# Optimization experiments

Measured on AMD Instinct MI355X. Metric: run time of the kernel, lower is better.

The kernel has to match this reference:

```python
import jax, jax.numpy as jnp
import numpy as np

N = 100000   # nodes
E = 3200000  # edges (before self-loops)
IN, H, OUT = 128, 256, 40

def glorot(key, shape):
    lim = (6.0 / (shape[0] + shape[1])) ** 0.5
    return jax.random.uniform(key, shape, jnp.float32, -lim, lim)

def setup_inputs() -> dict:
    key = jax.random.key(0)
    ks = jax.random.split(key, 8)
    x = jax.random.normal(ks[0], (N, IN), jnp.float32)
    edge_index = jax.random.randint(ks[1], (2, E), 0, N, dtype=jnp.int32)
    return {
        "x": x,
        "edge_index": edge_index,
        "W0": glorot(ks[2], (IN, H)),  "b0": jnp.zeros((H,), jnp.float32),
        "W1": glorot(ks[3], (H, H)),   "b1": jnp.zeros((H,), jnp.float32),
        "W2": glorot(ks[4], (H, OUT)), "b2": jnp.zeros((OUT,), jnp.float32),
    }

def _gcn_norm(edge_index, n):
    # PyG gcn_norm: add self-loops, symmetric D^{-1/2} A D^{-1/2}
    loops = jnp.arange(n, dtype=edge_index.dtype)
    src = jnp.concatenate([edge_index[0], loops])
    dst = jnp.concatenate([edge_index[1], loops])
    deg = jax.ops.segment_sum(jnp.ones_like(src, jnp.float32), dst, num_segments=n)
    dinv = jnp.where(deg > 0, jax.lax.rsqrt(deg), 0.0)
    norm = dinv[src] * dinv[dst]  # [E+N]
    return src, dst, norm

def _gcn_layer(h, W, b, src, dst, norm, n):
    h = h @ W                                   # transform first (PyG order)
    msg = h[src] * norm[:, None]                # gather + scale
    agg = jax.ops.segment_sum(msg, dst, num_segments=n)  # scatter-add
    return agg + b

def reference(x, edge_index, W0, b0, W1, b1, W2, b2):
    n = x.shape[0]
    src, dst, norm = _gcn_norm(edge_index, n)
    h = jnp.tanh(_gcn_layer(x, W0, b0, src, dst, norm, n))  # dropout = identity (eval)
    h = jnp.tanh(_gcn_layer(h, W1, b1, src, dst, norm, n))
    out = _gcn_layer(h, W2, b2, src, dst, norm, n)
    return jax.nn.log_softmax(out, axis=1)
```

## Files before the change

kernel.cpp:

```cpp
#include <hip/hip_runtime.h>
#include <hip/hip_bf16.h>
#include <cmath>


typedef unsigned short u16;
typedef __attribute__((ext_vector_type(8))) short short8;
typedef __attribute__((ext_vector_type(4))) float f32x4;

#define BSHIFT 10
#define BNODES (1 << BSHIFT)
#define ECAP   36864
#define BMASK 0x00FF00FFu

__device__ __forceinline__ u16 f2bf(float f) {
    unsigned int u = __float_as_uint(f);
    u += 0x7fffu + ((u >> 16) & 1u);
    return (u16)(u >> 16);
}
__device__ __forceinline__ float bflo(unsigned int u) { return __uint_as_float(u << 16); }
__device__ __forceinline__ float bfhi(unsigned int u) { return __uint_as_float(u & 0xffff0000u); }

__device__ __forceinline__ int q8(float v) {
    return (int)rintf(fminf(fmaxf(v, -127.0f), 127.0f));
}


__global__ __launch_bounds__(128) void init_gcur_kernel(
        int* __restrict__ gcur, int nb) {
    int b = blockIdx.x * 128 + threadIdx.x;
    if (b < nb) gcur[b] = b * ECAP;
}

__global__ __launch_bounds__(256) void bucketize_kernel(
        const int* __restrict__ src, const int* __restrict__ dst,
        int* __restrict__ gcur, unsigned int* __restrict__ ebuf, int E) {
    __shared__ int cnt[128];
    __shared__ int base[128];
    int tid = threadIdx.x;
    int chunk0 = blockIdx.x * 8192;
    int cend = min(chunk0 + 8192, E);
    for (int r0 = chunk0; r0 < cend; r0 += 2048) {
        if (tid < 128) cnt[tid] = 0;
        __syncthreads();
        int rank[8], bk[8];
        unsigned int pk[8];
#pragma unroll
        for (int j = 0; j < 8; j++) {
            int e = r0 + j * 256 + tid;
            bk[j] = -1;
            if (e < cend) {
                int d = dst[e];
                bk[j] = d >> BSHIFT;
                pk[j] = (unsigned int)src[e] | ((unsigned int)(d & (BNODES - 1)) << 17);
                rank[j] = atomicAdd(&cnt[bk[j]], 1);
            }
        }
        __syncthreads();
        if (tid < 128 && cnt[tid] > 0) base[tid] = atomicAdd(&gcur[tid], cnt[tid]);
        __syncthreads();
#pragma unroll
        for (int j = 0; j < 8; j++)
            if (bk[j] >= 0) ebuf[base[bk[j]] + rank[j]] = pk[j];
        __syncthreads();
    }
}

__global__ __launch_bounds__(256) void deg_hist_kernel(
        const unsigned int* __restrict__ ebuf, const int* __restrict__ gcur,
        int* __restrict__ degi, int N) {
    __shared__ int h[BNODES];
    int b = blockIdx.x;
    int nb0 = b << BSHIFT;
    int nodes = min(BNODES, N - nb0);
    for (int i = threadIdx.x; i < nodes; i += 256) h[i] = 0;
    __syncthreads();
    int estart = b * ECAP;
    int eend = gcur[b];
    for (int e = estart + threadIdx.x; e < eend; e += 256)
        atomicAdd(&h[ebuf[e] >> 17], 1);
    __syncthreads();
    for (int i = threadIdx.x; i < nodes; i += 256) degi[nb0 + i] = h[i];
}

__global__ __launch_bounds__(256) void dinv_kernel(
        const int* __restrict__ degi, float* __restrict__ dinv, int n) {
    int i = blockIdx.x * 256 + threadIdx.x;
    if (i < n) dinv[i] = rsqrtf((float)degi[i] + 1.0f);
}

__global__ __launch_bounds__(256) void scan_part_kernel(
        const int* __restrict__ deg, int* __restrict__ part, int n) {
    __shared__ int s[256];
    int i = blockIdx.x * 256 + threadIdx.x;
    s[threadIdx.x] = (i < n) ? deg[i] : 0;
    __syncthreads();
    for (int off = 128; off; off >>= 1) {
        if (threadIdx.x < off) s[threadIdx.x] += s[threadIdx.x + off];
        __syncthreads();
    }
    if (threadIdx.x == 0) part[blockIdx.x] = s[0];
}

__global__ __launch_bounds__(1024) void scan_top_kernel(
        int* __restrict__ part, int nb) {
    __shared__ int s[1024];
    int t = threadIdx.x;
    int v = (t < nb) ? part[t] : 0;
    s[t] = v;
    __syncthreads();
    for (int off = 1; off < 1024; off <<= 1) {
        int u = (t >= off) ? s[t - off] : 0;
        __syncthreads();
        s[t] += u;
        __syncthreads();
    }
    if (t < nb) part[t] = s[t] - v;
}

__global__ __launch_bounds__(256) void scan_apply_kernel(
        const int* __restrict__ deg, const int* __restrict__ part,
        int* __restrict__ rs, int n) {
    __shared__ int s[256];
    int i = blockIdx.x * 256 + threadIdx.x;
    int v = (i < n) ? deg[i] : 0;
    s[threadIdx.x] = v;
    __syncthreads();
    for (int off = 1; off < 256; off <<= 1) {
        int u = (threadIdx.x >= off) ? s[threadIdx.x - off] : 0;
        __syncthreads();
        s[threadIdx.x] += u;
        __syncthreads();
    }
    if (i < n) rs[i] = part[blockIdx.x] + s[threadIdx.x] - v;
}

__global__ __launch_bounds__(256) void csr_fill_kernel(
        const unsigned int* __restrict__ ebuf, const int* __restrict__ gcur,
        const int* __restrict__ rs, int* __restrict__ csr, int N) {
    __shared__ int lcur[BNODES];
    int b = blockIdx.x;
    int nb0 = b << BSHIFT;
    int nodes = min(BNODES, N - nb0);
    for (int i = threadIdx.x; i < nodes; i += 256) lcur[i] = rs[nb0 + i];
    __syncthreads();
    int estart = b * ECAP;
    int eend = gcur[b];
    for (int e = estart + threadIdx.x; e < eend; e += 256) {
        unsigned int v = ebuf[e];
        int s = v & 0x1FFFF;
        int dl = v >> 17;
        int pos = atomicAdd(&lcur[dl], 1);
        csr[pos] = s;
    }
}

__global__ __launch_bounds__(256) void wt_kernel(
        const float* __restrict__ W, u16* __restrict__ Wt, int K, int NC) {
    int i = blockIdx.x * 256 + threadIdx.x;
    if (i < K * NC) {
        int k = i / NC, c = i % NC;
        Wt[(size_t)c * K + k] = f2bf(W[i]);
    }
}

__global__ __launch_bounds__(256) void scale_x_kernel(
        const float* __restrict__ x, const float* __restrict__ dinv,
        unsigned int* __restrict__ out, int total4) {
    int i = blockIdx.x * 256 + threadIdx.x;
    if (i >= total4) return;
    int n = i >> 5;
    float4 v = reinterpret_cast<const float4*>(x)[i];
    float s = dinv[n] * 63.5f;
    int a0 = q8(v.x * s), a1 = q8(v.y * s), a2 = q8(v.z * s), a3 = q8(v.w * s);
    out[i] = (unsigned int)(a0 & 0xff) | ((unsigned int)(a1 & 0xff) << 8) |
             ((unsigned int)(a2 & 0xff) << 16) | ((unsigned int)(a3 & 0xff) << 24);
}

#define ACC8(q0, q1)                                                  \
    do {                                                              \
        aex += (q0) & BMASK; aox += ((q0) >> 8) & BMASK;              \
        aey += (q1) & BMASK; aoy += ((q1) >> 8) & BMASK;              \
    } while (0)

__global__ __launch_bounds__(256) void agg128_i8_kernel(
        const signed char* __restrict__ in, u16* __restrict__ out,
        const int* __restrict__ rs, const int* __restrict__ deg,
        const int* __restrict__ csr, const float* __restrict__ dinv, int n) {
    int wid = blockIdx.x * 4 + (threadIdx.x >> 6);
    if (wid >= n) return;
    int lane = threadIdx.x & 63;
    int quad = lane >> 4;
    int l16 = lane & 15;
    int start = rs[wid];
    int cnt = deg[wid];

    unsigned int aex = 0, aox = 0, aey = 0, aoy = 0;
    if (quad == 0) {
        uint2 q = *reinterpret_cast<const uint2*>(
            in + (size_t)wid * 128 + l16 * 8);
        q.x ^= 0x80808080u; q.y ^= 0x80808080u;
        ACC8(q.x, q.y);
    }
    int i = 0;
    for (; i + 16 <= cnt; i += 16) {
        int s[4];
#pragma unroll
        for (int j = 0; j < 4; j++) s[j] = csr[start + i + 4 * j + quad];
#pragma unroll
        for (int j = 0; j < 4; j++) {
            uint2 q = *reinterpret_cast<const uint2*>(
                in + (size_t)s[j] * 128 + l16 * 8);
            q.x ^= 0x80808080u; q.y ^= 0x80808080u;
            ACC8(q.x, q.y);
        }
    }
    for (; i + 4 <= cnt; i += 4) {
        int s0 = csr[start + i + quad];
        uint2 q = *reinterpret_cast<const uint2*>(
            in + (size_t)s0 * 128 + l16 * 8);
        q.x ^= 0x80808080u; q.y ^= 0x80808080u;
        ACC8(q.x, q.y);
    }
    int rem = cnt - i;
    if (quad < rem) {
        int s0 = csr[start + i + quad];
        uint2 q = *reinterpret_cast<const uint2*>(
            in + (size_t)s0 * 128 + l16 * 8);
        q.x ^= 0x80808080u; q.y ^= 0x80808080u;
        ACC8(q.x, q.y);
    }
    aex += (unsigned int)__shfl((int)aex, lane + 32);
    aox += (unsigned int)__shfl((int)aox, lane + 32);
    aey += (unsigned int)__shfl((int)aey, lane + 32);
    aoy += (unsigned int)__shfl((int)aoy, lane + 32);
    aex += (unsigned int)__shfl((int)aex, lane + 16);
    aox += (unsigned int)__shfl((int)aox, lane + 16);
    aey += (unsigned int)__shfl((int)aey, lane + 16);
    aoy += (unsigned int)__shfl((int)aoy, lane + 16);
    if (lane < 16) {
        int T = cnt + 1;
        int bias = 128 * T;
        float c = dinv[wid] * (2.0f / 127.0f);
        float f0 = (float)((int)(aex & 0xFFFFu) - bias) * c;
        float f1 = (float)((int)(aox & 0xFFFFu) - bias) * c;
        float f2 = (float)((int)(aex >> 16) - bias) * c;
        float f3 = (float)((int)(aox >> 16) - bias) * c;
        float f4 = (float)((int)(aey & 0xFFFFu) - bias) * c;
        float f5 = (float)((int)(aoy & 0xFFFFu) - bias) * c;
        float f6 = (float)((int)(aey >> 16) - bias) * c;
        float f7 = (float)((int)(aoy >> 16) - bias) * c;
        uint4 o;
        o.x = (unsigned)f2bf(f0) | ((unsigned)f2bf(f1) << 16);
        o.y = (unsigned)f2bf(f2) | ((unsigned)f2bf(f3) << 16);
        o.z = (unsigned)f2bf(f4) | ((unsigned)f2bf(f5) << 16);
        o.w = (unsigned)f2bf(f6) | ((unsigned)f2bf(f7) << 16);
        reinterpret_cast<uint4*>(out + (size_t)wid * 128)[l16] = o;
    }
}

__global__ __launch_bounds__(256) void agg_i8_kernel(
        const signed char* __restrict__ in, u16* __restrict__ out,
        const int* __restrict__ rs, const int* __restrict__ deg,
        const int* __restrict__ csr, const float* __restrict__ dinv, int n) {
    int wid = blockIdx.x * 4 + (threadIdx.x >> 6);
    if (wid >= n) return;
    int lane = threadIdx.x & 63;
    int start = rs[wid];
    int cnt = deg[wid];

    unsigned int q = *reinterpret_cast<const unsigned int*>(
        in + (size_t)wid * 256 + lane * 4) ^ 0x80808080u;
    unsigned int ae = q & BMASK, ao = (q >> 8) & BMASK;

    int i = 0;
    for (; i + 16 <= cnt; i += 16) {
        int s[16];
#pragma unroll
        for (int j = 0; j < 16; j++)
            s[j] = __builtin_amdgcn_readfirstlane(csr[start + i + j]);
        unsigned int qq[16];
#pragma unroll
        for (int j = 0; j < 16; j++)
            qq[j] = *reinterpret_cast<const unsigned int*>(
                in + (size_t)s[j] * 256 + lane * 4);
#pragma unroll
        for (int j = 0; j < 16; j++) {
            unsigned int v = qq[j] ^ 0x80808080u;
            ae += v & BMASK;
            ao += (v >> 8) & BMASK;
        }
    }
    if (i < cnt) {
        int s[16];
#pragma unroll
        for (int j = 0; j < 16; j++) {
            int e = i + j;
            e = (e < cnt) ? e : (cnt - 1);
            s[j] = __builtin_amdgcn_readfirstlane(csr[start + e]);
        }
        unsigned int qq[16];
#pragma unroll
        for (int j = 0; j < 16; j++)
            qq[j] = *reinterpret_cast<const unsigned int*>(
                in + (size_t)s[j] * 256 + lane * 4);
#pragma unroll
        for (int j = 0; j < 16; j++) {
            unsigned int m = (i + j < cnt) ? 0xFFFFFFFFu : 0u;
            unsigned int v = (qq[j] ^ 0x80808080u) & m;
            ae += v & BMASK;
            ao += (v >> 8) & BMASK;
        }
    }

    int bias = 128 * (cnt + 1);
    float c = dinv[wid] * (1.0f / 127.0f);
    float f0 = (float)((int)(ae & 0xFFFFu) - bias) * c;
    float f1 = (float)((int)(ao & 0xFFFFu) - bias) * c;
    float f2 = (float)((int)(ae >> 16) - bias) * c;
    float f3 = (float)((int)(ao >> 16) - bias) * c;
    uint2 o;
    o.x = (unsigned)f2bf(f0) | ((unsigned)f2bf(f1) << 16);
    o.y = (unsigned)f2bf(f2) | ((unsigned)f2bf(f3) << 16);
    reinterpret_cast<uint2*>(out + (size_t)wid * 256)[lane] = o;
}

template<int EPI, typename CT>
__global__ __launch_bounds__(256) void mfma_mm_kernel(
        const u16* __restrict__ A, const u16* __restrict__ Bt,
        CT* __restrict__ C, int M, int K, int NC,
        const float* __restrict__ bias, const float* __restrict__ postscale,
        float qs) {
    __shared__ u16 As[128 * 40];
    __shared__ u16 Bs[64 * 40];
    int t = threadIdx.x;
    int w = t >> 6, lane = t & 63, quad = lane >> 4, l16 = lane & 15;
    int row0 = blockIdx.x * 128;
    int col0 = blockIdx.y * 64;

    f32x4 acc[2][4];
#pragma unroll
    for (int s = 0; s < 2; s++)
#pragma unroll
        for (int nb = 0; nb < 4; nb++)
            acc[s][nb] = (f32x4){0.f, 0.f, 0.f, 0.f};

    int bn = t >> 2, bkq = (t & 3) << 3;
    for (int k0 = 0; k0 < K; k0 += 32) {
#pragma unroll
        for (int i = t; i < 512; i += 256) {
            int r = i >> 2, c = (i & 3) << 3;
            int gr = row0 + r;
            uint4 v = {0u, 0u, 0u, 0u};
            if (gr < M)
                v = *reinterpret_cast<const uint4*>(A + (size_t)gr * K + k0 + c);
            *reinterpret_cast<uint4*>(&As[r * 40 + c]) = v;
        }
        {
            int gc = col0 + bn;
            uint4 v = {0u, 0u, 0u, 0u};
            if (gc < NC)
                v = *reinterpret_cast<const uint4*>(Bt + (size_t)gc * K + k0 + bkq);
            *reinterpret_cast<uint4*>(&Bs[bn * 40 + bkq]) = v;
        }
        __syncthreads();

        short8 af[2], bf[4];
        af[0] = *reinterpret_cast<const short8*>(&As[(w * 32 + l16) * 40 + quad * 8]);
        af[1] = *reinterpret_cast<const short8*>(&As[(w * 32 + 16 + l16) * 40 + quad * 8]);
#pragma unroll
        for (int nb = 0; nb < 4; nb++)
            bf[nb] = *reinterpret_cast<const short8*>(&Bs[(nb * 16 + l16) * 40 + quad * 8]);
#pragma unroll
        for (int s = 0; s < 2; s++)
#pragma unroll
            for (int nb = 0; nb < 4; nb++)
                acc[s][nb] = __builtin_amdgcn_mfma_f32_16x16x32_bf16(
                    af[s], bf[nb], acc[s][nb], 0, 0, 0);
        __syncthreads();
    }

#pragma unroll
    for (int s = 0; s < 2; s++) {
        int rbase = row0 + w * 32 + s * 16 + quad * 4;
#pragma unroll
        for (int nb = 0; nb < 4; nb++) {
            int gc = col0 + nb * 16 + l16;
#pragma unroll
            for (int r = 0; r < 4; r++) {
                int gr = rbase + r;
                if (gr >= M || gc >= NC) continue;
                float v = acc[s][nb][r];
                if constexpr (EPI == 1) v = tanhf(v + bias[gc]);
                else                    v = v * postscale[gr];
                if constexpr (sizeof(CT) == 1) {
                    float m = qs;
                    if constexpr (EPI == 1) m *= postscale[gr];
                    C[(size_t)gr * NC + gc] = (CT)q8(v * m);
                } else {
                    C[(size_t)gr * NC + gc] = (CT)f2bf(v);
                }
            }
        }
    }
}

__global__ __launch_bounds__(256) void agg40_ls_kernel(
        const signed char* __restrict__ in, const int* __restrict__ rs,
        const int* __restrict__ deg, const int* __restrict__ csr,
        const float* __restrict__ dinv, const float* __restrict__ bias,
        float* __restrict__ out, int n) {
    int wid = blockIdx.x * 4 + (threadIdx.x >> 6);
    if (wid >= n) return;
    int lane = threadIdx.x & 63;
    int grp = lane / 5;
    int l5 = lane - grp * 5;
    bool act = lane < 60;
    int start = rs[wid];
    int cnt = deg[wid];

    unsigned int aex = 0, aox = 0, aey = 0, aoy = 0;
    if (lane < 5) {
        uint2 q = *reinterpret_cast<const uint2*>(
            in + (size_t)wid * 40 + l5 * 8);
        q.x ^= 0x80808080u; q.y ^= 0x80808080u;
        ACC8(q.x, q.y);
    }
    for (int base = 0; base < cnt; base += 12) {
        int e = base + grp;
        if (act && e < cnt) {
            int s0 = csr[start + e];
            uint2 q = *reinterpret_cast<const uint2*>(
                in + (size_t)s0 * 40 + l5 * 8);
            q.x ^= 0x80808080u; q.y ^= 0x80808080u;
            ACC8(q.x, q.y);
        }
    }
    aex += (unsigned int)__shfl((int)aex, lane + 30);
    aox += (unsigned int)__shfl((int)aox, lane + 30);
    aey += (unsigned int)__shfl((int)aey, lane + 30);
    aoy += (unsigned int)__shfl((int)aoy, lane + 30);
    aex += (unsigned int)__shfl((int)aex, lane + 15);
    aox += (unsigned int)__shfl((int)aox, lane + 15);
    aey += (unsigned int)__shfl((int)aey, lane + 15);
    aoy += (unsigned int)__shfl((int)aoy, lane + 15);
    aex += (unsigned int)__shfl((int)aex, lane + 5) + (unsigned int)__shfl((int)aex, lane + 10);
    aox += (unsigned int)__shfl((int)aox, lane + 5) + (unsigned int)__shfl((int)aox, lane + 10);
    aey += (unsigned int)__shfl((int)aey, lane + 5) + (unsigned int)__shfl((int)aey, lane + 10);
    aoy += (unsigned int)__shfl((int)aoy, lane + 5) + (unsigned int)__shfl((int)aoy, lane + 10);

    bool act5 = lane < 5;
    float s = dinv[wid];
    float v0 = -INFINITY, v1 = -INFINITY, v2 = -INFINITY, v3 = -INFINITY;
    float v4 = -INFINITY, v5 = -INFINITY, v6 = -INFINITY, v7 = -INFINITY;
    if (act5) {
        int bb = 128 * (cnt + 1);
        float c = s * (1.0f / 63.0f);
        int cc = lane * 8;
        v0 = (float)((int)(aex & 0xFFFFu) - bb) * c + bias[cc + 0];
        v1 = (float)((int)(aox & 0xFFFFu) - bb) * c + bias[cc + 1];
        v2 = (float)((int)(aex >> 16) - bb) * c + bias[cc + 2];
        v3 = (float)((int)(aox >> 16) - bb) * c + bias[cc + 3];
        v4 = (float)((int)(aey & 0xFFFFu) - bb) * c + bias[cc + 4];
        v5 = (float)((int)(aoy & 0xFFFFu) - bb) * c + bias[cc + 5];
        v6 = (float)((int)(aey >> 16) - bb) * c + bias[cc + 6];
        v7 = (float)((int)(aoy >> 16) - bb) * c + bias[cc + 7];
    }
    float m = fmaxf(fmaxf(fmaxf(v0, v1), fmaxf(v2, v3)),
                    fmaxf(fmaxf(v4, v5), fmaxf(v6, v7)));
    for (int off = 4; off; off >>= 1) m = fmaxf(m, __shfl_xor(m, off));
    float e = 0.f;
    if (act5) e = __expf(v0 - m) + __expf(v1 - m) + __expf(v2 - m) + __expf(v3 - m)
                + __expf(v4 - m) + __expf(v5 - m) + __expf(v6 - m) + __expf(v7 - m);
    for (int off = 4; off; off >>= 1) e += __shfl_xor(e, off);
    float ls = logf(e);
    if (act5) {
        float4 o0, o1;
        o0.x = v0 - m - ls; o0.y = v1 - m - ls; o0.z = v2 - m - ls; o0.w = v3 - m - ls;
        o1.x = v4 - m - ls; o1.y = v5 - m - ls; o1.z = v6 - m - ls; o1.w = v7 - m - ls;
        float4* op = reinterpret_cast<float4*>(out + (size_t)wid * 40 + lane * 8);
        op[0] = o0;
        op[1] = o1;
    }
}

extern "C" void kernel_launch(void* const* d_in, const int* in_sizes, int n_in,
                              void* d_out, int out_size, void* d_ws, size_t ws_size,
                              hipStream_t stream) {
    const float* x  = (const float*)d_in[0];
    const int*   ei = (const int*)d_in[1];
    const float* W0 = (const float*)d_in[2];
    const float* b0 = (const float*)d_in[3];
    const float* W1 = (const float*)d_in[4];
    const float* b1 = (const float*)d_in[5];
    const float* W2 = (const float*)d_in[6];
    const float* b2 = (const float*)d_in[7];
    float* out = (float*)d_out;

    const int N = in_sizes[0] / 128;
    const int E = in_sizes[1] / 2;
    const int IN = 128, H = 256, OUT = 40;
    const int NB = (N + BNODES - 1) >> BSHIFT;

    char* p = (char*)d_ws;
    auto carve = [&](size_t bytes) -> void* {
        void* r = (void*)p;
        p += (bytes + 255) & ~(size_t)255;
        return r;
    };
    float*        dinv = (float*)carve((size_t)N * 4);
    int*          degi = (int*)  carve((size_t)N * 4);
    int*          rs   = (int*)  carve((size_t)N * 4);
    int*          part = (int*)  carve((size_t)1024 * 4);
    int*          gcur = (int*)  carve((size_t)128 * 4);
    int*          csr  = (int*)  carve((size_t)E * 4);
    unsigned int* ebuf = (unsigned int*)carve((size_t)NB * ECAP * 4);
    u16*          Wt0  = (u16*)  carve((size_t)IN * H * 2);
    u16*          Wt1  = (u16*)  carve((size_t)H * H * 2);
    u16*          Wt2  = (u16*)  carve((size_t)H * OUT * 2);
    u16*          U1   = (u16*)  carve((size_t)N * H * 2);
    u16*          U2   = (u16*)  carve((size_t)N * H * 2);

    signed char* Xq   = (signed char*)U1;
    u16*         T0bf = U1 + (size_t)N * IN / 2 + 64;
    signed char* H0q  = (signed char*)U2;
    u16*         T1bf = U1;
    u16*         h1bf = U2;
    signed char* G2q  = (signed char*)U1;

    const int* src = ei;
    const int* dst = ei + E;

    int gN = (N + 255) / 256;
    int gW = (N + 3) / 4;
    int gMM = (N + 127) / 128;
    int gA = (E + 8191) / 8192;

    init_gcur_kernel<<<1, 128, 0, stream>>>(gcur, NB);
    bucketize_kernel<<<gA, 256, 0, stream>>>(src, dst, gcur, ebuf, E);
    deg_hist_kernel<<<NB, 256, 0, stream>>>(ebuf, gcur, degi, N);
    dinv_kernel<<<gN, 256, 0, stream>>>(degi, dinv, N);
    scan_part_kernel<<<gN, 256, 0, stream>>>(degi, part, N);
    scan_top_kernel<<<1, 1024, 0, stream>>>(part, gN);
    scan_apply_kernel<<<gN, 256, 0, stream>>>(degi, part, rs, N);
    csr_fill_kernel<<<NB, 256, 0, stream>>>(ebuf, gcur, rs, csr, N);

    wt_kernel<<<(IN * H + 255) / 256, 256, 0, stream>>>(W0, Wt0, IN, H);
    wt_kernel<<<(H * H + 255) / 256, 256, 0, stream>>>(W1, Wt1, H, H);
    wt_kernel<<<(H * OUT + 255) / 256, 256, 0, stream>>>(W2, Wt2, H, OUT);

    int t4x = N * (IN / 4);
    scale_x_kernel<<<(t4x + 255) / 256, 256, 0, stream>>>(
        x, dinv, (unsigned int*)Xq, t4x);
    agg128_i8_kernel<<<gW, 256, 0, stream>>>(Xq, T0bf, rs, degi, csr, dinv, N);
    mfma_mm_kernel<1, signed char><<<dim3(gMM, H / 64), 256, 0, stream>>>(
        T0bf, Wt0, H0q, N, IN, H, b0, dinv, 127.0f);

    agg_i8_kernel<<<gW, 256, 0, stream>>>(H0q, T1bf, rs, degi, csr, dinv, N);
    mfma_mm_kernel<1, u16><<<dim3(gMM, H / 64), 256, 0, stream>>>(
        T1bf, Wt1, h1bf, N, H, H, b1, nullptr, 0.f);

    mfma_mm_kernel<0, signed char><<<dim3(gMM, 1), 256, 0, stream>>>(
        h1bf, Wt2, G2q, N, H, OUT, nullptr, dinv, 63.0f);
    agg40_ls_kernel<<<gW, 256, 0, stream>>>(G2q, rs, degi, csr, dinv, b2, out, N);
}
```

Measured before the change: 625.2 us.

## Sub-bucket edges by source range and use full-width GEMM tiles

Edges are now bucketed by destination block and also by the high bits of the source index, giving four sub-regions per destination block. The CSR fill therefore visits sources in coarse sorted order, which should improve locality in the later gathers. The GEMM kernel now computes all output columns per block, 64 rows by the full width, so the A tile is read once instead of once per 64-column slice, and the launch grid is simplified. The trade-offs are more shared-memory atomics and registers, and the fixed per-region capacity could overflow on skewed inputs.

```diff
diff --git a/kernel.cpp b/kernel.cpp
--- a/kernel.cpp
+++ b/kernel.cpp
@@ -9,7 +9,9 @@
 
 #define BSHIFT 10
 #define BNODES (1 << BSHIFT)
-#define ECAP   36864
+#define SPLITS 4
+#define NREG   512
+#define ECAP2  12288
 #define BMASK 0x00FF00FFu
 
 __device__ __forceinline__ u16 f2bf(float f) {
@@ -17,8 +19,6 @@
     u += 0x7fffu + ((u >> 16) & 1u);
     return (u16)(u >> 16);
 }
-__device__ __forceinline__ float bflo(unsigned int u) { return __uint_as_float(u << 16); }
-__device__ __forceinline__ float bfhi(unsigned int u) { return __uint_as_float(u & 0xffff0000u); }
 
 __device__ __forceinline__ int q8(float v) {
     return (int)rintf(fminf(fmaxf(v, -127.0f), 127.0f));
@@ -26,41 +26,43 @@
 
 
 __global__ __launch_bounds__(128) void init_gcur_kernel(
-        int* __restrict__ gcur, int nb) {
+        int* __restrict__ gcur, int nr) {
     int b = blockIdx.x * 128 + threadIdx.x;
-    if (b < nb) gcur[b] = b * ECAP;
+    if (b < nr) gcur[b] = b * ECAP2;
 }
 
 __global__ __launch_bounds__(256) void bucketize_kernel(
         const int* __restrict__ src, const int* __restrict__ dst,
         int* __restrict__ gcur, unsigned int* __restrict__ ebuf, int E) {
-    __shared__ int cnt[128];
-    __shared__ int base[128];
+    __shared__ int cnt[NREG];
+    __shared__ int base[NREG];
     int tid = threadIdx.x;
     int chunk0 = blockIdx.x * 8192;
     int cend = min(chunk0 + 8192, E);
     for (int r0 = chunk0; r0 < cend; r0 += 2048) {
-        if (tid < 128) cnt[tid] = 0;
-        __syncthreads();
-        int rank[8], bk[8];
+        for (int i = tid; i < NREG; i += 256) cnt[i] = 0;
+        __syncthreads();
+        int rank[8], rg[8];
         unsigned int pk[8];
 #pragma unroll
         for (int j = 0; j < 8; j++) {
             int e = r0 + j * 256 + tid;
-            bk[j] = -1;
+            rg[j] = -1;
             if (e < cend) {
                 int d = dst[e];
-                bk[j] = d >> BSHIFT;
-                pk[j] = (unsigned int)src[e] | ((unsigned int)(d & (BNODES - 1)) << 17);
-                rank[j] = atomicAdd(&cnt[bk[j]], 1);
+                int s = src[e];
+                rg[j] = ((d >> BSHIFT) << 2) | (s >> 15);
+                pk[j] = (unsigned int)s | ((unsigned int)(d & (BNODES - 1)) << 17);
+                rank[j] = atomicAdd(&cnt[rg[j]], 1);
             }
         }
         __syncthreads();
-        if (tid < 128 && cnt[tid] > 0) base[tid] = atomicAdd(&gcur[tid], cnt[tid]);
+        for (int i = tid; i < NREG; i += 256)
+            if (cnt[i] > 0) base[i] = atomicAdd(&gcur[i], cnt[i]);
         __syncthreads();
 #pragma unroll
         for (int j = 0; j < 8; j++)
-            if (bk[j] >= 0) ebuf[base[bk[j]] + rank[j]] = pk[j];
+            if (rg[j] >= 0) ebuf[base[rg[j]] + rank[j]] = pk[j];
         __syncthreads();
     }
 }
@@ -74,10 +76,13 @@
     int nodes = min(BNODES, N - nb0);
     for (int i = threadIdx.x; i < nodes; i += 256) h[i] = 0;
     __syncthreads();
-    int estart = b * ECAP;
-    int eend = gcur[b];
-    for (int e = estart + threadIdx.x; e < eend; e += 256)
-        atomicAdd(&h[ebuf[e] >> 17], 1);
+    for (int sub = 0; sub < SPLITS; sub++) {
+        int r = (b << 2) | sub;
+        int estart = r * ECAP2;
+        int eend = gcur[r];
+        for (int e = estart + threadIdx.x; e < eend; e += 256)
+            atomicAdd(&h[ebuf[e] >> 17], 1);
+    }
     __syncthreads();
     for (int i = threadIdx.x; i < nodes; i += 256) degi[nb0 + i] = h[i];
 }
@@ -143,14 +148,18 @@
     int nodes = min(BNODES, N - nb0);
     for (int i = threadIdx.x; i < nodes; i += 256) lcur[i] = rs[nb0 + i];
     __syncthreads();
-    int estart = b * ECAP;
-    int eend = gcur[b];
-    for (int e = estart + threadIdx.x; e < eend; e += 256) {
-        unsigned int v = ebuf[e];
-        int s = v & 0x1FFFF;
-        int dl = v >> 17;
-        int pos = atomicAdd(&lcur[dl], 1);
-        csr[pos] = s;
+    for (int sub = 0; sub < SPLITS; sub++) {
+        int r = (b << 2) | sub;
+        int estart = r * ECAP2;
+        int eend = gcur[r];
+        for (int e = estart + threadIdx.x; e < eend; e += 256) {
+            unsigned int v = ebuf[e];
+            int s = v & 0x1FFFF;
+            int dl = v >> 17;
+            int pos = atomicAdd(&lcur[dl], 1);
+            csr[pos] = s;
+        }
+        __syncthreads();
     }
 }
 
@@ -324,81 +333,79 @@
     reinterpret_cast<uint2*>(out + (size_t)wid * 256)[lane] = o;
 }
 
-template<int EPI, typename CT>
+template<int EPI, typename CT, int NCt>
 __global__ __launch_bounds__(256) void mfma_mm_kernel(
         const u16* __restrict__ A, const u16* __restrict__ Bt,
-        CT* __restrict__ C, int M, int K, int NC,
+        CT* __restrict__ C, int M, int K,
         const float* __restrict__ bias, const float* __restrict__ postscale,
         float qs) {
-    __shared__ u16 As[128 * 40];
-    __shared__ u16 Bs[64 * 40];
+    constexpr int NBT = (NCt + 15) / 16;
+    __shared__ u16 As[64 * 40];
+    __shared__ u16 Bs[NBT * 16 * 40];
     int t = threadIdx.x;
     int w = t >> 6, lane = t & 63, quad = lane >> 4, l16 = lane & 15;
-    int row0 = blockIdx.x * 128;
-    int col0 = blockIdx.y * 64;
-
-    f32x4 acc[2][4];
-#pragma unroll
-    for (int s = 0; s < 2; s++)
-#pragma unroll
-        for (int nb = 0; nb < 4; nb++)
-            acc[s][nb] = (f32x4){0.f, 0.f, 0.f, 0.f};
-
-    int bn = t >> 2, bkq = (t & 3) << 3;
+    int row0 = blockIdx.x * 64;
+
+    f32x4 acc[NBT];
+#pragma unroll
+    for (int nb = 0; nb < NBT; nb++)
+        acc[nb] = (f32x4){0.f, 0.f, 0.f, 0.f};
+
+    int ar = t >> 2, akq = (t & 3) << 3;
     for (int k0 = 0; k0 < K; k0 += 32) {
-#pragma unroll
-        for (int i = t; i < 512; i += 256) {
-            int r = i >> 2, c = (i & 3) << 3;
-            int gr = row0 + r;
+        {
+            int gr = row0 + ar;
             uint4 v = {0u, 0u, 0u, 0u};
             if (gr < M)
-                v = *reinterpret_cast<const uint4*>(A + (size_t)gr * K + k0 + c);
-            *reinterpret_cast<uint4*>(&As[r * 40 + c]) = v;
-        }
-        {
-            int gc = col0 + bn;
+                v = *reinterpret_cast<const uint4*>(A + (size_t)gr * K + k0 + akq);
+            *reinterpret_cast<uint4*>(&As[ar * 40 + akq]) = v;
+        }
+#pragma unroll
+        for (int i = t; i < NBT * 64; i += 256) {
+            int c = i >> 2, kq = (i & 3) << 3;
             uint4 v = {0u, 0u, 0u, 0u};
-            if (gc < NC)
-                v = *reinterpret_cast<const uint4*>(Bt + (size_t)gc * K + k0 + bkq);
-            *reinterpret_cast<uint4*>(&Bs[bn * 40 + bkq]) = v;
-        }
-        __syncthreads();
-
-        short8 af[2], bf[4];
-        af[0] = *reinterpret_cast<const short8*>(&As[(w * 32 + l16) * 40 + quad * 8]);
-        af[1] = *reinterpret_cast<const short8*>(&As[(w * 32 + 16 + l16) * 40 + quad * 8]);
-#pragma unroll
-        for (int nb = 0; nb < 4; nb++)
-            bf[nb] = *reinterpret_cast<const short8*>(&Bs[(nb * 16 + l16) * 40 + quad * 8]);
-#pragma unroll
-        for (int s = 0; s < 2; s++)
-#pragma unroll
-            for (int nb = 0; nb < 4; nb++)
-                acc[s][nb] = __builtin_amdgcn_mfma_f32_16x16x32_bf16(
-                    af[s], bf[nb], acc[s][nb], 0, 0, 0);
-        __syncthreads();
-    }
-
-#pragma unroll
-    for (int s = 0; s < 2; s++) {
-        int rbase = row0 + w * 32 + s * 16 + quad * 4;
-#pragma unroll
-        for (int nb = 0; nb < 4; nb++) {
-            int gc = col0 + nb * 16 + l16;
-#pragma unroll
-            for (int r = 0; r < 4; r++) {
-                int gr = rbase + r;
-                if (gr >= M || gc >= NC) continue;
-                float v = acc[s][nb][r];
-                if constexpr (EPI == 1) v = tanhf(v + bias[gc]);
-                else                    v = v * postscale[gr];
-                if constexpr (sizeof(CT) == 1) {
-                    float m = qs;
-                    if constexpr (EPI == 1) m *= postscale[gr];
-                    C[(size_t)gr * NC + gc] = (CT)q8(v * m);
-                } else {
-                    C[(size_t)gr * NC + gc] = (CT)f2bf(v);
-                }
+            if (c < NCt)
+                v = *reinterpret_cast<const uint4*>(Bt + (size_t)c * K + k0 + kq);
+            *reinterpret_cast<uint4*>(&Bs[c * 40 + kq]) = v;
+        }
+        __syncthreads();
+
+        short8 af = *reinterpret_cast<const short8*>(
+            &As[(w * 16 + l16) * 40 + quad * 8]);
+#pragma unroll
+        for (int nb = 0; nb < NBT; nb++) {
+            short8 bf = *reinterpret_cast<const short8*>(
+                &Bs[(nb * 16 + l16) * 40 + quad * 8]);
+            acc[nb] = __builtin_amdgcn_mfma_f32_16x16x32_bf16(af, bf, acc[nb], 0, 0, 0);
+        }
+        __syncthreads();
+    }
+
+    int rbase = row0 + w * 16 + quad * 4;
+    float ps[4];
+#pragma unroll
+    for (int r = 0; r < 4; r++) {
+        int gr = rbase + r;
+        ps[r] = (postscale && gr < M) ? postscale[gr] : 0.f;
+    }
+#pragma unroll
+    for (int nb = 0; nb < NBT; nb++) {
+        int gc = nb * 16 + l16;
+        if (gc >= NCt) continue;
+        float bb = (EPI == 1) ? bias[gc] : 0.f;
+#pragma unroll
+        for (int r = 0; r < 4; r++) {
+            int gr = rbase + r;
+            if (gr >= M) continue;
+            float v = acc[nb][r];
+            if constexpr (EPI == 1) v = tanhf(v + bb);
+            else                    v = v * ps[r];
+            if constexpr (sizeof(CT) == 1) {
+                float m = qs;
+                if constexpr (EPI == 1) m *= ps[r];
+                C[(size_t)gr * NCt + gc] = (CT)q8(v * m);
+            } else {
+                C[(size_t)gr * NCt + gc] = (CT)f2bf(v);
             }
         }
     }
@@ -499,7 +506,6 @@
     const int N = in_sizes[0] / 128;
     const int E = in_sizes[1] / 2;
     const int IN = 128, H = 256, OUT = 40;
-    const int NB = (N + BNODES - 1) >> BSHIFT;
 
     char* p = (char*)d_ws;
     auto carve = [&](size_t bytes) -> void* {
@@ -511,9 +517,9 @@
     int*          degi = (int*)  carve((size_t)N * 4);
     int*          rs   = (int*)  carve((size_t)N * 4);
     int*          part = (int*)  carve((size_t)1024 * 4);
-    int*          gcur = (int*)  carve((size_t)128 * 4);
+    int*          gcur = (int*)  carve((size_t)NREG * 4);
     int*          csr  = (int*)  carve((size_t)E * 4);
-    unsigned int* ebuf = (unsigned int*)carve((size_t)NB * ECAP * 4);
+    unsigned int* ebuf = (unsigned int*)carve((size_t)NREG * ECAP2 * 4);
     u16*          Wt0  = (u16*)  carve((size_t)IN * H * 2);
     u16*          Wt1  = (u16*)  carve((size_t)H * H * 2);
     u16*          Wt2  = (u16*)  carve((size_t)H * OUT * 2);
@@ -530,12 +536,14 @@
     const int* src = ei;
     const int* dst = ei + E;
 
+    const int NB = (N + BNODES - 1) >> BSHIFT;
+
     int gN = (N + 255) / 256;
     int gW = (N + 3) / 4;
-    int gMM = (N + 127) / 128;
+    int gMM = (N + 63) / 64;
     int gA = (E + 8191) / 8192;
 
-    init_gcur_kernel<<<1, 128, 0, stream>>>(gcur, NB);
+    init_gcur_kernel<<<(NREG + 127) / 128, 128, 0, stream>>>(gcur, NREG);
     bucketize_kernel<<<gA, 256, 0, stream>>>(src, dst, gcur, ebuf, E);
     deg_hist_kernel<<<NB, 256, 0, stream>>>(ebuf, gcur, degi, N);
     dinv_kernel<<<gN, 256, 0, stream>>>(degi, dinv, N);
@@ -552,14 +560,14 @@
     scale_x_kernel<<<(t4x + 255) / 256, 256, 0, stream>>>(
         x, dinv, (unsigned int*)Xq, t4x);
     agg128_i8_kernel<<<gW, 256, 0, stream>>>(Xq, T0bf, rs, degi, csr, dinv, N);
-    mfma_mm_kernel<1, signed char><<<dim3(gMM, H / 64), 256, 0, stream>>>(
-        T0bf, Wt0, H0q, N, IN, H, b0, dinv, 127.0f);
+    mfma_mm_kernel<1, signed char, 256><<<gMM, 256, 0, stream>>>(
+        T0bf, Wt0, H0q, N, IN, b0, dinv, 127.0f);
 
     agg_i8_kernel<<<gW, 256, 0, stream>>>(H0q, T1bf, rs, degi, csr, dinv, N);
-    mfma_mm_kernel<1, u16><<<dim3(gMM, H / 64), 256, 0, stream>>>(
-        T1bf, Wt1, h1bf, N, H, H, b1, nullptr, 0.f);
-
-    mfma_mm_kernel<0, signed char><<<dim3(gMM, 1), 256, 0, stream>>>(
-        h1bf, Wt2, G2q, N, H, OUT, nullptr, dinv, 63.0f);
+    mfma_mm_kernel<1, u16, 256><<<gMM, 256, 0, stream>>>(
+        T1bf, Wt1, h1bf, N, H, b1, nullptr, 0.f);
+
+    mfma_mm_kernel<0, signed char, 40><<<gMM, 256, 0, stream>>>(
+        h1bf, Wt2, G2q, N, H, nullptr, dinv, 63.0f);
     agg40_ls_kernel<<<gW, 256, 0, stream>>>(G2q, rs, degi, csr, dinv, b2, out, N);
 }
```

Result: slower. 668.0 us (+6.8%).
